# Kernel optimization log

Measured on AMD Instinct MI355X. Metric: run time of the kernel, lower is better.

The kernel has to match this reference:

```python
import jax, jax.numpy as jnp
import numpy as np

N_HEAD = 16
D_QK = 128
D_V = 128
D_MODEL = 2048
BATCH = 2
SEQ = 2048


def alibi_slopes(n_head):
    # standard ALiBi slopes: 2^(-8*i/n_head) for i = 1..n_head
    return jnp.asarray(2.0 ** (-8.0 * np.arange(1, n_head + 1) / n_head), dtype=jnp.float32)


def setup_inputs() -> dict:
    key = jax.random.key(0)
    k1, k2, k3, k4, k5 = jax.random.split(key, 5)
    x = jax.random.normal(k1, (BATCH, SEQ, D_MODEL), dtype=jnp.float32)
    # causal attention mask (1 = keep, 0 = masked), broadcast over heads
    causal = jnp.tril(jnp.ones((SEQ, SEQ), dtype=bool))
    attention_mask = jnp.broadcast_to(causal, (BATCH, 1, SEQ, SEQ))
    Wq = jax.random.normal(k2, (D_MODEL, N_HEAD * D_QK), dtype=jnp.float32) * (D_MODEL ** -0.5)
    Wk = jax.random.normal(k3, (D_MODEL, N_HEAD * D_QK), dtype=jnp.float32) * (D_MODEL ** -0.5)
    Wv = jax.random.normal(k4, (D_MODEL, N_HEAD * D_V), dtype=jnp.float32) * (D_MODEL ** -0.5)
    Wo = jax.random.normal(k5, (N_HEAD * D_V, D_MODEL), dtype=jnp.float32) * ((N_HEAD * D_V) ** -0.5)
    return {"x": x, "attention_mask": attention_mask, "Wq": Wq, "Wk": Wk, "Wv": Wv, "Wo": Wo}


def reference(x, attention_mask, Wq, Wk, Wv, Wo):
    B, S, _ = x.shape
    scale = D_QK ** -0.5
    q = (x @ Wq).reshape(B, S, N_HEAD, D_QK).transpose(0, 2, 1, 3)  # [B,H,S,dqk]
    k = (x @ Wk).reshape(B, S, N_HEAD, D_QK).transpose(0, 2, 1, 3)
    v = (x @ Wv).reshape(B, S, N_HEAD, D_V).transpose(0, 2, 1, 3)
    scores = jnp.einsum('bhid,bhjd->bhij', q, k) * scale  # [B,H,S,S]
    # ALiBi bias: slope_h * (j - i), negative penalty for distant past keys
    pos = jnp.arange(S, dtype=jnp.float32)
    rel = pos[None, :] - pos[:, None]  # [S,S]
    slopes = alibi_slopes(N_HEAD)
    scores = scores + slopes[None, :, None, None] * rel[None, None, :, :]
    scores = jnp.where(attention_mask, scores, jnp.float32(-jnp.inf))
    attn = jax.nn.softmax(scores, axis=-1)
    out = jnp.einsum('bhij,bhjd->bhid', attn, v)  # [B,H,S,dv]
    out = out.transpose(0, 2, 1, 3).reshape(B, S, N_HEAD * D_V)
    return out @ Wo
```

## Files before the change

kernel.cpp:

```cpp
#include <hip/hip_runtime.h>
#include <cstdint>

typedef unsigned short u16;
typedef __attribute__((ext_vector_type(4))) u16 u16x4;
typedef __attribute__((ext_vector_type(8))) u16 u16x8;
typedef __attribute__((ext_vector_type(8))) __bf16 bf16x8;
typedef __attribute__((ext_vector_type(4))) float f32x4;

#define LOG2E 1.44269504088896340736f

static __device__ __forceinline__ u16 f2bf(float f) {
  unsigned u = __builtin_bit_cast(unsigned, f);
  u += 0x7fffu + ((u >> 16) & 1u);
  return (u16)(u >> 16);
}
static __device__ __forceinline__ float bf2f(u16 v) {
  unsigned u = ((unsigned)v) << 16;
  return __builtin_bit_cast(float, u);
}


static __device__ __forceinline__ void gload16(const u16* g, u16* l) {
  __builtin_amdgcn_global_load_lds(
      (__attribute__((address_space(1))) void*)(uintptr_t)g,
      (__attribute__((address_space(3))) void*)(uintptr_t)l, 16, 0, 0);
}

static __device__ __forceinline__ bf16x8 lds_bf8(const void* p) {
  return __builtin_bit_cast(bf16x8, *(const u16x8*)p);
}

__global__ __launch_bounds__(256) void cast_x_kernel(const float* __restrict__ src,
                                                     u16* __restrict__ dst) {
  int i = (blockIdx.x * 256 + threadIdx.x) * 4;
  float4 v = *(const float4*)(src + i);
  u16x4 r = {f2bf(v.x), f2bf(v.y), f2bf(v.z), f2bf(v.w)};
  *(u16x4*)(dst + i) = r;
}

__global__ __launch_bounds__(256) void transpose_w4_kernel(const float* Wq, const float* Wk,
                                                           const float* Wv, const float* Wo,
                                                           u16* Wqt, u16* Wkt, u16* Wvt,
                                                           u16* Wot) {
  const float* src = blockIdx.z == 0 ? Wq : (blockIdx.z == 1 ? Wk : (blockIdx.z == 2 ? Wv : Wo));
  u16* dst = blockIdx.z == 0 ? Wqt : (blockIdx.z == 1 ? Wkt : (blockIdx.z == 2 ? Wvt : Wot));
  __shared__ float tile[32][33];
  const int n0 = blockIdx.x * 32, k0 = blockIdx.y * 32;
  const int tx = threadIdx.x & 31, ty = threadIdx.x >> 5;
#pragma unroll
  for (int r = 0; r < 4; ++r) {
    int row = r * 8 + ty;
    tile[row][tx] = src[(size_t)(k0 + row) * 2048 + n0 + tx];
  }
  __syncthreads();
#pragma unroll
  for (int r = 0; r < 4; ++r) {
    int row = r * 8 + ty;
    dst[(size_t)(n0 + row) * 2048 + k0 + tx] = f2bf(tile[tx][row]);
  }
}

#define GSTAGE(TILE, KH, BUF)                                                        \
  do {                                                                               \
    const int bk = (TILE) * 64 + (KH) * 32;                                          \
    u16* as_ = &lds[((BUF) * 2 + (KH)) * 8192];                                      \
    u16* bs_ = &lds[32768 + ((BUF) * 2 + (KH)) * BSLOT];                             \
    gload16(&A[(size_t)(m0 + sr) * 2048 + bk + scu], as_ + tid * 8);                 \
    gload16(&A[(size_t)(m0 + 128 + sr) * 2048 + bk + scu], as_ + 4096 + tid * 8);    \
    gload16(&Bt[(size_t)(n0 + sr) * 2048 + bk + scu], bs_ + tid * 8);                \
    if constexpr (BN == 256)                                                         \
      gload16(&Bt[(size_t)(n0 + 128 + sr) * 2048 + bk + scu], bs_ + 4096 + tid * 8); \
  } while (0)

#define GPH(BUF, KH, STAGE_STMT, VMLIT)                                              \
  do {                                                                               \
    const u16* as_ = &lds[((BUF) * 2 + (KH)) * 8192];                                \
    const u16* bs_ = &lds[32768 + ((BUF) * 2 + (KH)) * BSLOT];                       \
    bf16x8 af[8], bq[NF];                                                            \
    _Pragma("unroll") for (int mf = 0; mf < 8; ++mf) {                               \
      const int ar = wm * 128 + mf * 16 + l16;                                       \
      af[mf] = lds_bf8(&as_[(ar * 32 + lg * 8) ^ xsw]);                              \
    }                                                                                \
    _Pragma("unroll") for (int nf = 0; nf < NF; ++nf) {                              \
      const int br = wn * (BN / 4) + nf * 16 + l16;                                  \
      bq[nf] = lds_bf8(&bs_[(br * 32 + lg * 8) ^ xsw]);                              \
    }                                                                                \
    STAGE_STMT;                                                                      \
    asm volatile("s_barrier" ::: "memory");                                          \
    __builtin_amdgcn_s_setprio(1);                                                   \
    _Pragma("unroll") for (int mf = 0; mf < 8; ++mf)                                 \
        _Pragma("unroll") for (int nf = 0; nf < NF; ++nf) acc[mf][nf] =              \
            __builtin_amdgcn_mfma_f32_16x16x32_bf16(af[mf], bq[nf], acc[mf][nf], 0, 0, 0); \
    __builtin_amdgcn_s_setprio(0);                                                   \
    __builtin_amdgcn_sched_barrier(0);                                               \
    asm volatile("s_waitcnt vmcnt(" #VMLIT ")\n\ts_barrier" ::: "memory");           \
  } while (0)

template <int BN, int MODE>
__device__ __forceinline__ void gemm_dp(const u16* __restrict__ A, const u16* __restrict__ Bt,
                                        void* __restrict__ Cout, int m0, int n0) {
  constexpr int BSLOT = BN * 32;
  constexpr int NF = BN / 64;
  __shared__ u16 lds[32768 + 4 * BSLOT];
  const int tid = threadIdx.x, lane = tid & 63, w = tid >> 6;
  const int wm = w >> 2, wn = w & 3;
  const int l16 = lane & 15, lg = lane >> 4;
  const int sr = tid >> 2;
  const int scu = (((tid & 3) ^ ((tid >> 2) & 3))) * 8;
  const int xsw = (l16 & 3) * 8;

  f32x4 acc[8][NF];
#pragma unroll
  for (int i = 0; i < 8; ++i)
#pragma unroll
    for (int j = 0; j < NF; ++j) acc[i][j] = f32x4{0.f, 0.f, 0.f, 0.f};

  GSTAGE(0, 0, 0);
  GSTAGE(0, 1, 0);
  GSTAGE(1, 0, 1);
  if constexpr (BN == 256) {
    asm volatile("s_waitcnt vmcnt(8)\n\ts_barrier" ::: "memory");
    for (int m2 = 0; m2 < 30; m2 += 2) {
      GPH(0, 0, GSTAGE(m2 + 1, 1, 1), 8);
      GPH(0, 1, GSTAGE(m2 + 2, 0, 0), 8);
      GPH(1, 0, GSTAGE(m2 + 2, 1, 0), 8);
      GPH(1, 1, GSTAGE(m2 + 3, 0, 1), 8);
    }
    GPH(0, 0, GSTAGE(31, 1, 1), 8);
    GPH(0, 1, (void)0, 4);
    GPH(1, 0, (void)0, 0);
    GPH(1, 1, (void)0, 0);
  } else {
    asm volatile("s_waitcnt vmcnt(6)\n\ts_barrier" ::: "memory");
    for (int m2 = 0; m2 < 30; m2 += 2) {
      GPH(0, 0, GSTAGE(m2 + 1, 1, 1), 6);
      GPH(0, 1, GSTAGE(m2 + 2, 0, 0), 6);
      GPH(1, 0, GSTAGE(m2 + 2, 1, 0), 6);
      GPH(1, 1, GSTAGE(m2 + 3, 0, 1), 6);
    }
    GPH(0, 0, GSTAGE(31, 1, 1), 6);
    GPH(0, 1, (void)0, 3);
    GPH(1, 0, (void)0, 0);
    GPH(1, 1, (void)0, 0);
  }

  constexpr int WNS = BN / 4;
#pragma unroll
  for (int mf = 0; mf < 8; ++mf)
#pragma unroll
    for (int nf = 0; nf < NF; ++nf)
#pragma unroll
      for (int r = 0; r < 4; ++r) {
        const int row = m0 + wm * 128 + mf * 16 + lg * 4 + r;
        const int col = n0 + wn * WNS + nf * 16 + l16;
        const float v = acc[mf][nf][r];
        if constexpr (MODE == 0) {
          size_t off =
              (((size_t)(row >> 11) * 16 + (col >> 7)) * 2048 + (row & 2047)) * 128 + (col & 127);
          ((u16*)Cout)[off] = f2bf(v);
        } else if constexpr (MODE == 2) {
          size_t off =
              (((size_t)(col >> 11) * 16 + (row >> 7)) * 128 + (row & 127)) * 2048 + (col & 2047);
          ((u16*)Cout)[off] = f2bf(v);
        } else {
          ((float*)Cout)[(size_t)row * 2048 + col] = v;
        }
      }
}

__global__ __launch_bounds__(512, 2) void qkproj_kernel(const u16* xb, const u16* Wqt,
                                                        const u16* Wkt, u16* Qb, u16* Kb) {
  const int n0g = blockIdx.y * 256;
  const u16* Bt = (n0g < 2048) ? Wqt : Wkt;
  u16* dst = (n0g < 2048) ? Qb : Kb;
  gemm_dp<256, 0>(xb, Bt, dst, blockIdx.x * 256, n0g & 2047);
}

__global__ __launch_bounds__(512, 2) void vt_kernel(const u16* Wvt, const u16* xb, u16* Vb) {
  gemm_dp<128, 2>(Wvt, xb, Vb, blockIdx.x * 256, blockIdx.y * 128);
}

__global__ __launch_bounds__(512, 2) void out_kernel(const u16* OA, const u16* Wot, float* C) {
  gemm_dp<128, 1>(OA, Wot, C, blockIdx.x * 256, blockIdx.y * 128);
}

__global__ __launch_bounds__(256) void attn_kernel(const u16* __restrict__ Q,
                                                   const u16* __restrict__ Kg,
                                                   const u16* __restrict__ Vg,
                                                   u16* __restrict__ O,
                                                   u16* __restrict__ Opart,
                                                   float* __restrict__ Lp) {
  const int tid = threadIdx.x, lane = tid & 63, w = tid >> 6;
  const int l16 = lane & 15, lg = lane >> 4;

  const int u = blockIdx.x >> 5, bh = blockIdx.x & 31;
  int tile, st0, st1, slot = 0;
  bool multi = false;
  if (u == 0) { tile = 17; st0 = 0; st1 = 18; }
  else if (u == 1) { tile = 16; st0 = 0; st1 = 17; }
  else if (u < 30) {
    multi = true;
    const int c = u - 2, ti = c >> 1, ch = c & 1;
    tile = 31 - ti;
    const int s = tile + 1, half = (s + 1) >> 1;
    st0 = ch ? half : 0;
    st1 = ch ? s : half;
    slot = bh * 28 + c;
  } else { tile = 45 - u; st0 = 0; st1 = tile + 1; }

  const int q0 = tile * 64;
  const int h = bh & 15, b = bh >> 4;
  const float sl2 = exp2f(-0.5f * (float)(h + 1)) * LOG2E;
  const float sc2 = 0.08838834764831845f * LOG2E;

  __shared__ u16 Kl[64 * 128];
  __shared__ u16 Vl[128 * 64];
  __shared__ u16 Pl[64 * 64];

  const size_t qk_base = (size_t)bh * 2048 * 128;
  const size_t v_base = (size_t)bh * 128 * 2048;

  const u16* kgs = Kg + qk_base + (size_t)(tid >> 4) * 128 + (((tid & 15) ^ ((tid >> 4) & 7)) * 8);
  const u16* vgs = Vg + v_base + (size_t)(tid >> 3) * 2048 + (((tid & 7) ^ ((tid >> 3) & 7)) * 8);

#define STAGEKV(STX)                                                        \
  do {                                                                      \
    const int j0s = (STX)*64;                                               \
    _Pragma("unroll") for (int s = 0; s < 4; ++s) {                         \
      gload16(kgs + (size_t)(j0s + s * 16) * 128, Kl + s * 2048 + tid * 8); \
      gload16(vgs + (size_t)s * 32 * 2048 + j0s, Vl + s * 2048 + tid * 8);  \
    }                                                                       \
  } while (0)

  STAGEKV(st0);

  bf16x8 qf[4];
#pragma unroll
  for (int ks = 0; ks < 4; ++ks)
    qf[ks] = lds_bf8(&Q[qk_base + (size_t)(q0 + w * 16 + l16) * 128 + ks * 32 + lg * 8]);

  f32x4 oacc[8];
#pragma unroll
  for (int j = 0; j < 8; ++j) oacc[j] = f32x4{0.f, 0.f, 0.f, 0.f};
  float lsum0 = 0.f, lsum1 = 0.f;

  float ab4[4], rsl[4];
#pragma unroll
  for (int nf = 0; nf < 4; ++nf)
    ab4[nf] = (float)(st0 * 64 + nf * 16 - q0 - w * 16 - l16) * sl2;
#pragma unroll
  for (int r = 0; r < 4; ++r) rsl[r] = (float)(lg * 4 + r) * sl2;
  const float abinc = 64.0f * sl2;
  const int qrow = w * 16 + l16;
  const int dmaskb = lg * 4 - w * 16 - l16;

  __syncthreads();

#define ASTEP(MASKED)                                                                     \
  do {                                                                                    \
    f32x4 sacc[4];                                                                        \
    _Pragma("unroll") for (int j = 0; j < 4; ++j) sacc[j] = f32x4{0.f, 0.f, 0.f, 0.f};    \
    __builtin_amdgcn_s_setprio(1);                                                        \
    _Pragma("unroll") for (int ks = 0; ks < 4; ++ks) {                                    \
      bf16x8 kf[4];                                                                       \
      _Pragma("unroll") for (int nf = 0; nf < 4; ++nf) {                                  \
        int j = nf * 16 + l16;                                                            \
        kf[nf] = lds_bf8((char*)Kl + ((j * 256 + (ks * 32 + lg * 8) * 2) ^ ((j & 7) << 4))); \
      }                                                                                   \
      _Pragma("unroll") for (int nf = 0; nf < 4; ++nf) sacc[nf] =                         \
          __builtin_amdgcn_mfma_f32_16x16x32_bf16(kf[nf], qf[ks], sacc[nf], 0, 0, 0);     \
    }                                                                                     \
    __builtin_amdgcn_s_setprio(0);                                                        \
    _Pragma("unroll") for (int nf = 0; nf < 4; ++nf) {                                    \
      float pvv[4];                                                                       \
      _Pragma("unroll") for (int r = 0; r < 4; ++r) {                                     \
        float s2 = fmaf(sacc[nf][r], sc2, ab4[nf] + rsl[r]);                              \
        float pv = exp2f(s2);                                                             \
        if (MASKED) pv = (nf * 16 + r + dmaskb <= 0) ? pv : 0.f;                          \
        pvv[r] = pv;                                                                      \
      }                                                                                   \
      ab4[nf] += abinc;                                                                   \
      lsum0 += pvv[0] + pvv[1];                                                           \
      lsum1 += pvv[2] + pvv[3];                                                           \
      unsigned w0_, w1_;                                                                  \
      asm("v_cvt_pk_bf16_f32 %0, %1, %2" : "=v"(w0_) : "v"(pvv[0]), "v"(pvv[1]));         \
      asm("v_cvt_pk_bf16_f32 %0, %1, %2" : "=v"(w1_) : "v"(pvv[2]), "v"(pvv[3]));         \
      uint2 pw_{w0_, w1_};                                                                \
      *(uint2*)((char*)Pl + ((qrow * 128 + (nf * 16 + lg * 4) * 2) ^ ((qrow & 7) << 4))) = pw_; \
    }                                                                                     \
    __builtin_amdgcn_s_setprio(1);                                                        \
    _Pragma("unroll") for (int ks = 0; ks < 2; ++ks) {                                    \
      bf16x8 pf =                                                                         \
          lds_bf8((char*)Pl + ((qrow * 128 + (ks * 32 + lg * 8) * 2) ^ ((qrow & 7) << 4))); \
      _Pragma("unroll") for (int nf = 0; nf < 8; ++nf) {                                  \
        int d = nf * 16 + l16;                                                            \
        bf16x8 vf =                                                                       \
            lds_bf8((char*)Vl + ((d * 128 + (ks * 32 + lg * 8) * 2) ^ ((d & 7) << 4)));   \
        oacc[nf] = __builtin_amdgcn_mfma_f32_16x16x32_bf16(pf, vf, oacc[nf], 0, 0, 0);    \
      }                                                                                   \
    }                                                                                     \
    __builtin_amdgcn_s_setprio(0);                                                        \
    if (st + 1 < st1) {                                                                   \
      __syncthreads();                                                                    \
      STAGEKV(st + 1);                                                                    \
      __syncthreads();                                                                    \
    }                                                                                     \
  } while (0)

  int st = st0;
  const int bulk_end = min(st1, tile);
  for (; st < bulk_end; ++st) ASTEP(false);
  for (; st < st1; ++st) ASTEP(true);
#undef STAGEKV
#undef ASTEP

  float lr = lsum0 + lsum1;
  lr += __shfl_xor(lr, 16, 64);
  lr += __shfl_xor(lr, 32, 64);

  if (multi) {
    if (lg == 0) Lp[(size_t)slot * 64 + qrow] = lr;
#pragma unroll
    for (int r = 0; r < 4; ++r) {
      const int row = w * 16 + lg * 4 + r;
#pragma unroll
      for (int nf = 0; nf < 8; ++nf)
        Opart[((size_t)slot * 64 + row) * 128 + nf * 16 + l16] = f2bf(oacc[nf][r]);
    }
  } else {
#pragma unroll
    for (int r = 0; r < 4; ++r) {
      const float inv = 1.0f / __shfl(lr, lg * 4 + r, 64);
      const int srow = q0 + w * 16 + lg * 4 + r;
#pragma unroll
      for (int nf = 0; nf < 8; ++nf)
        O[((size_t)b * 2048 + srow) * 2048 + h * 128 + nf * 16 + l16] = f2bf(oacc[nf][r] * inv);
    }
  }
}

__global__ __launch_bounds__(256) void combine_kernel(const u16* __restrict__ Opart,
                                                      const float* __restrict__ Lp,
                                                      u16* __restrict__ O) {
  const int bx = blockIdx.x;
  const int bh = bx / 14, ti = bx % 14;
  const int tile = 31 - ti;
  const int slot0 = bh * 28 + ti * 2, slot1 = slot0 + 1;
  const int b = bh >> 4, h = bh & 15;
  const int q0 = tile * 64;
  const int tid = threadIdx.x;
  const int colg = (tid & 15) * 8, rowb = tid >> 4;
#pragma unroll
  for (int rr = 0; rr < 4; ++rr) {
    const int row = rowb + rr * 16;
    const float l0 = Lp[(size_t)slot0 * 64 + row];
    const float l1 = Lp[(size_t)slot1 * 64 + row];
    const float inv = 1.0f / (l0 + l1);
    u16x8 p0 = *(const u16x8*)&Opart[((size_t)slot0 * 64 + row) * 128 + colg];
    u16x8 p1 = *(const u16x8*)&Opart[((size_t)slot1 * 64 + row) * 128 + colg];
    u16x8 o;
#pragma unroll
    for (int e = 0; e < 8; ++e) o[e] = f2bf((bf2f(p0[e]) + bf2f(p1[e])) * inv);
    *(u16x8*)&O[((size_t)b * 2048 + q0 + row) * 2048 + h * 128 + colg] = o;
  }
}

extern "C" void kernel_launch(void* const* d_in, const int* in_sizes, int n_in, void* d_out,
                              int out_size, void* d_ws, size_t ws_size, hipStream_t stream) {
  const float* x = (const float*)d_in[0];
  const float* Wq = (const float*)d_in[2];
  const float* Wk = (const float*)d_in[3];
  const float* Wv = (const float*)d_in[4];
  const float* Wo = (const float*)d_in[5];
  char* ws = (char*)d_ws;

  const size_t MB = 1048576;
  u16* xb = (u16*)(ws);
  u16* Qb = (u16*)(ws + 16 * MB);
  u16* Kb = (u16*)(ws + 32 * MB);
  u16* Vb = (u16*)(ws + 48 * MB);
  u16* Wqt = (u16*)(ws + 64 * MB);
  u16* Wkt = (u16*)(ws + 72 * MB);
  u16* Wvt = (u16*)(ws + 80 * MB);
  u16* Wot = (u16*)(ws + 88 * MB);
  u16* OA = xb;
  u16* Opart = (u16*)(ws + 72 * MB);
  float* Lpf = (float*)(ws + 72 * MB + 896ull * 64 * 128 * 2);

  cast_x_kernel<<<8192, 256, 0, stream>>>(x, xb);
  transpose_w4_kernel<<<dim3(64, 64, 4), 256, 0, stream>>>(Wq, Wk, Wv, Wo, Wqt, Wkt, Wvt, Wot);
  qkproj_kernel<<<dim3(16, 16), 512, 0, stream>>>(xb, Wqt, Wkt, Qb, Kb);
  vt_kernel<<<dim3(8, 32), 512, 0, stream>>>(Wvt, xb, Vb);
  attn_kernel<<<dim3(1472), 256, 0, stream>>>(Qb, Kb, Vb, OA, Opart, Lpf);
  combine_kernel<<<dim3(448), 256, 0, stream>>>(Opart, Lpf, OA);
  out_kernel<<<dim3(16, 16), 512, 0, stream>>>(OA, Wot, (float*)d_out);
}
```

Before: 251.9 us.

## Give BN=128 GEMMs a three-stage 64-wide K pipeline with 8-way swizzle

The QK projection kernel is specialised inline for BN=256. The V-transpose and output-projection GEMMs move to a new gemm_dp2 path. That path stages full 64-wide K tiles into a three-buffer ring (144KB LDS) with an 8-column XOR swizzle, and each wave issues 32 MFMAs per phase instead of 16. The goal is fewer barriers per K step and deeper prefetch to hide global latency. The cost is occupancy: launch bounds drop to one block per CU because of the larger LDS footprint.

```diff
diff --git a/kernel.cpp b/kernel.cpp
--- a/kernel.cpp
+++ b/kernel.cpp
@@ -64,44 +64,48 @@
   do {                                                                               \
     const int bk = (TILE) * 64 + (KH) * 32;                                          \
     u16* as_ = &lds[((BUF) * 2 + (KH)) * 8192];                                      \
-    u16* bs_ = &lds[32768 + ((BUF) * 2 + (KH)) * BSLOT];                             \
+    u16* bs_ = &lds[32768 + ((BUF) * 2 + (KH)) * 8192];                              \
     gload16(&A[(size_t)(m0 + sr) * 2048 + bk + scu], as_ + tid * 8);                 \
     gload16(&A[(size_t)(m0 + 128 + sr) * 2048 + bk + scu], as_ + 4096 + tid * 8);    \
     gload16(&Bt[(size_t)(n0 + sr) * 2048 + bk + scu], bs_ + tid * 8);                \
-    if constexpr (BN == 256)                                                         \
-      gload16(&Bt[(size_t)(n0 + 128 + sr) * 2048 + bk + scu], bs_ + 4096 + tid * 8); \
+    gload16(&Bt[(size_t)(n0 + 128 + sr) * 2048 + bk + scu], bs_ + 4096 + tid * 8);   \
   } while (0)
 
 #define GPH(BUF, KH, STAGE_STMT, VMLIT)                                              \
   do {                                                                               \
     const u16* as_ = &lds[((BUF) * 2 + (KH)) * 8192];                                \
-    const u16* bs_ = &lds[32768 + ((BUF) * 2 + (KH)) * BSLOT];                       \
-    bf16x8 af[8], bq[NF];                                                            \
+    const u16* bs_ = &lds[32768 + ((BUF) * 2 + (KH)) * 8192];                        \
+    bf16x8 af[8], bq[4];                                                             \
     _Pragma("unroll") for (int mf = 0; mf < 8; ++mf) {                               \
       const int ar = wm * 128 + mf * 16 + l16;                                       \
       af[mf] = lds_bf8(&as_[(ar * 32 + lg * 8) ^ xsw]);                              \
     }                                                                                \
-    _Pragma("unroll") for (int nf = 0; nf < NF; ++nf) {                              \
-      const int br = wn * (BN / 4) + nf * 16 + l16;                                  \
+    _Pragma("unroll") for (int nf = 0; nf < 4; ++nf) {                               \
+      const int br = wn * 64 + nf * 16 + l16;                                        \
       bq[nf] = lds_bf8(&bs_[(br * 32 + lg * 8) ^ xsw]);                              \
     }                                                                                \
     STAGE_STMT;                                                                      \
     asm volatile("s_barrier" ::: "memory");                                          \
     __builtin_amdgcn_s_setprio(1);                                                   \
     _Pragma("unroll") for (int mf = 0; mf < 8; ++mf)                                 \
-        _Pragma("unroll") for (int nf = 0; nf < NF; ++nf) acc[mf][nf] =              \
+        _Pragma("unroll") for (int nf = 0; nf < 4; ++nf) acc[mf][nf] =               \
             __builtin_amdgcn_mfma_f32_16x16x32_bf16(af[mf], bq[nf], acc[mf][nf], 0, 0, 0); \
     __builtin_amdgcn_s_setprio(0);                                                   \
     __builtin_amdgcn_sched_barrier(0);                                               \
     asm volatile("s_waitcnt vmcnt(" #VMLIT ")\n\ts_barrier" ::: "memory");           \
   } while (0)
 
-template <int BN, int MODE>
-__device__ __forceinline__ void gemm_dp(const u16* __restrict__ A, const u16* __restrict__ Bt,
-                                        void* __restrict__ Cout, int m0, int n0) {
-  constexpr int BSLOT = BN * 32;
-  constexpr int NF = BN / 64;
-  __shared__ u16 lds[32768 + 4 * BSLOT];
+__global__ __launch_bounds__(512, 2) void qkproj_kernel(const u16* __restrict__ xb,
+                                                        const u16* __restrict__ Wqt,
+                                                        const u16* __restrict__ Wkt,
+                                                        u16* __restrict__ Qb,
+                                                        u16* __restrict__ Kb) {
+  const int n0g = blockIdx.y * 256;
+  const u16* Bt = (n0g < 2048) ? Wqt : Wkt;
+  u16* Cout = (n0g < 2048) ? Qb : Kb;
+  const u16* A = xb;
+  const int m0 = blockIdx.x * 256, n0 = n0g & 2047;
+  __shared__ u16 lds[65536];
   const int tid = threadIdx.x, lane = tid & 63, w = tid >> 6;
   const int wm = w >> 2, wn = w & 3;
   const int l16 = lane & 15, lg = lane >> 4;
@@ -109,56 +113,120 @@
   const int scu = (((tid & 3) ^ ((tid >> 2) & 3))) * 8;
   const int xsw = (l16 & 3) * 8;
 
-  f32x4 acc[8][NF];
+  f32x4 acc[8][4];
 #pragma unroll
   for (int i = 0; i < 8; ++i)
 #pragma unroll
-    for (int j = 0; j < NF; ++j) acc[i][j] = f32x4{0.f, 0.f, 0.f, 0.f};
+    for (int j = 0; j < 4; ++j) acc[i][j] = f32x4{0.f, 0.f, 0.f, 0.f};
 
   GSTAGE(0, 0, 0);
   GSTAGE(0, 1, 0);
   GSTAGE(1, 0, 1);
-  if constexpr (BN == 256) {
-    asm volatile("s_waitcnt vmcnt(8)\n\ts_barrier" ::: "memory");
-    for (int m2 = 0; m2 < 30; m2 += 2) {
-      GPH(0, 0, GSTAGE(m2 + 1, 1, 1), 8);
-      GPH(0, 1, GSTAGE(m2 + 2, 0, 0), 8);
-      GPH(1, 0, GSTAGE(m2 + 2, 1, 0), 8);
-      GPH(1, 1, GSTAGE(m2 + 3, 0, 1), 8);
-    }
-    GPH(0, 0, GSTAGE(31, 1, 1), 8);
-    GPH(0, 1, (void)0, 4);
-    GPH(1, 0, (void)0, 0);
-    GPH(1, 1, (void)0, 0);
-  } else {
-    asm volatile("s_waitcnt vmcnt(6)\n\ts_barrier" ::: "memory");
-    for (int m2 = 0; m2 < 30; m2 += 2) {
-      GPH(0, 0, GSTAGE(m2 + 1, 1, 1), 6);
-      GPH(0, 1, GSTAGE(m2 + 2, 0, 0), 6);
-      GPH(1, 0, GSTAGE(m2 + 2, 1, 0), 6);
-      GPH(1, 1, GSTAGE(m2 + 3, 0, 1), 6);
-    }
-    GPH(0, 0, GSTAGE(31, 1, 1), 6);
-    GPH(0, 1, (void)0, 3);
-    GPH(1, 0, (void)0, 0);
-    GPH(1, 1, (void)0, 0);
-  }
-
-  constexpr int WNS = BN / 4;
+  asm volatile("s_waitcnt vmcnt(8)\n\ts_barrier" ::: "memory");
+  for (int m2 = 0; m2 < 30; m2 += 2) {
+    GPH(0, 0, GSTAGE(m2 + 1, 1, 1), 8);
+    GPH(0, 1, GSTAGE(m2 + 2, 0, 0), 8);
+    GPH(1, 0, GSTAGE(m2 + 2, 1, 0), 8);
+    GPH(1, 1, GSTAGE(m2 + 3, 0, 1), 8);
+  }
+  GPH(0, 0, GSTAGE(31, 1, 1), 8);
+  GPH(0, 1, (void)0, 4);
+  GPH(1, 0, (void)0, 0);
+  GPH(1, 1, (void)0, 0);
+
 #pragma unroll
   for (int mf = 0; mf < 8; ++mf)
 #pragma unroll
-    for (int nf = 0; nf < NF; ++nf)
+    for (int nf = 0; nf < 4; ++nf)
 #pragma unroll
       for (int r = 0; r < 4; ++r) {
         const int row = m0 + wm * 128 + mf * 16 + lg * 4 + r;
-        const int col = n0 + wn * WNS + nf * 16 + l16;
+        const int col = n0 + wn * 64 + nf * 16 + l16;
+        size_t off =
+            (((size_t)(row >> 11) * 16 + (col >> 7)) * 2048 + (row & 2047)) * 128 + (col & 127);
+        Cout[off] = f2bf(acc[mf][nf][r]);
+      }
+}
+
+#define GSTAGE2(TILE, S)                                                             \
+  do {                                                                               \
+    const int bk2 = (TILE) * 64;                                                     \
+    u16* as_ = &lds[(S) * 16384];                                                    \
+    u16* bs_ = &lds[49152 + (S) * 8192];                                             \
+    gload16(pA2 + bk2, as_ + tid * 8);                                               \
+    gload16(pA2 + bk2 + (size_t)64 * 2048, as_ + 4096 + tid * 8);                    \
+    gload16(pA2 + bk2 + (size_t)128 * 2048, as_ + 8192 + tid * 8);                   \
+    gload16(pA2 + bk2 + (size_t)192 * 2048, as_ + 12288 + tid * 8);                  \
+    gload16(pB2 + bk2, bs_ + tid * 8);                                               \
+    gload16(pB2 + bk2 + (size_t)64 * 2048, bs_ + 4096 + tid * 8);                    \
+  } while (0)
+
+#define GPH2(S, STAGE_STMT, VMLIT)                                                   \
+  do {                                                                               \
+    const char* as_ = (const char*)&lds[(S) * 16384];                                \
+    const char* bs_ = (const char*)&lds[49152 + (S) * 8192];                         \
+    bf16x8 af[2][8], bq[2][2];                                                       \
+    _Pragma("unroll") for (int kh = 0; kh < 2; ++kh)                                 \
+        _Pragma("unroll") for (int mf = 0; mf < 8; ++mf) {                           \
+      const int ar = wm * 128 + mf * 16 + l16;                                       \
+      af[kh][mf] = lds_bf8(as_ + ((ar * 128 + (kh * 4 + lg) * 16) ^ ((l16 & 7) << 4))); \
+    }                                                                                \
+    _Pragma("unroll") for (int kh = 0; kh < 2; ++kh)                                 \
+        _Pragma("unroll") for (int nf = 0; nf < 2; ++nf) {                           \
+      const int br = wn * 32 + nf * 16 + l16;                                        \
+      bq[kh][nf] = lds_bf8(bs_ + ((br * 128 + (kh * 4 + lg) * 16) ^ ((l16 & 7) << 4))); \
+    }                                                                                \
+    STAGE_STMT;                                                                      \
+    asm volatile("s_barrier" ::: "memory");                                          \
+    __builtin_amdgcn_s_setprio(1);                                                   \
+    _Pragma("unroll") for (int kh = 0; kh < 2; ++kh)                                 \
+        _Pragma("unroll") for (int mf = 0; mf < 8; ++mf)                             \
+            _Pragma("unroll") for (int nf = 0; nf < 2; ++nf) acc[mf][nf] =           \
+                __builtin_amdgcn_mfma_f32_16x16x32_bf16(af[kh][mf], bq[kh][nf],      \
+                                                        acc[mf][nf], 0, 0, 0);      \
+    __builtin_amdgcn_s_setprio(0);                                                   \
+    __builtin_amdgcn_sched_barrier(0);                                               \
+    asm volatile("s_waitcnt vmcnt(" #VMLIT ")\n\ts_barrier" ::: "memory");           \
+  } while (0)
+
+template <int MODE>
+__device__ __forceinline__ void gemm_dp2(const u16* __restrict__ A, const u16* __restrict__ Bt,
+                                         void* __restrict__ Cout, int m0, int n0) {
+  __shared__ u16 lds[73728];
+  const int tid = threadIdx.x, lane = tid & 63, w = tid >> 6;
+  const int wm = w >> 2, wn = w & 3;
+  const int l16 = lane & 15, lg = lane >> 4;
+  const int scol2 = ((tid & 7) ^ ((tid >> 3) & 7)) * 8;
+  const u16* pA2 = A + (size_t)(m0 + (tid >> 3)) * 2048 + scol2;
+  const u16* pB2 = Bt + (size_t)(n0 + (tid >> 3)) * 2048 + scol2;
+
+  f32x4 acc[8][2];
+#pragma unroll
+  for (int i = 0; i < 8; ++i)
+#pragma unroll
+    for (int j = 0; j < 2; ++j) acc[i][j] = f32x4{0.f, 0.f, 0.f, 0.f};
+
+  GSTAGE2(0, 0);
+  GSTAGE2(1, 1);
+  asm volatile("s_waitcnt vmcnt(6)\n\ts_barrier" ::: "memory");
+  for (int t = 0; t < 30; t += 3) {
+    GPH2(0, GSTAGE2(t + 2, 2), 6);
+    GPH2(1, GSTAGE2(t + 3, 0), 6);
+    GPH2(2, GSTAGE2(t + 4, 1), 6);
+  }
+  GPH2(0, (void)0, 0);
+  GPH2(1, (void)0, 0);
+
+#pragma unroll
+  for (int mf = 0; mf < 8; ++mf)
+#pragma unroll
+    for (int nf = 0; nf < 2; ++nf)
+#pragma unroll
+      for (int r = 0; r < 4; ++r) {
+        const int row = m0 + wm * 128 + mf * 16 + lg * 4 + r;
+        const int col = n0 + wn * 32 + nf * 16 + l16;
         const float v = acc[mf][nf][r];
-        if constexpr (MODE == 0) {
-          size_t off =
-              (((size_t)(row >> 11) * 16 + (col >> 7)) * 2048 + (row & 2047)) * 128 + (col & 127);
-          ((u16*)Cout)[off] = f2bf(v);
-        } else if constexpr (MODE == 2) {
+        if constexpr (MODE == 2) {
           size_t off =
               (((size_t)(col >> 11) * 16 + (row >> 7)) * 128 + (row & 127)) * 2048 + (col & 2047);
           ((u16*)Cout)[off] = f2bf(v);
@@ -168,20 +236,12 @@
       }
 }
 
-__global__ __launch_bounds__(512, 2) void qkproj_kernel(const u16* xb, const u16* Wqt,
-                                                        const u16* Wkt, u16* Qb, u16* Kb) {
-  const int n0g = blockIdx.y * 256;
-  const u16* Bt = (n0g < 2048) ? Wqt : Wkt;
-  u16* dst = (n0g < 2048) ? Qb : Kb;
-  gemm_dp<256, 0>(xb, Bt, dst, blockIdx.x * 256, n0g & 2047);
-}
-
-__global__ __launch_bounds__(512, 2) void vt_kernel(const u16* Wvt, const u16* xb, u16* Vb) {
-  gemm_dp<128, 2>(Wvt, xb, Vb, blockIdx.x * 256, blockIdx.y * 128);
-}
-
-__global__ __launch_bounds__(512, 2) void out_kernel(const u16* OA, const u16* Wot, float* C) {
-  gemm_dp<128, 1>(OA, Wot, C, blockIdx.x * 256, blockIdx.y * 128);
+__global__ __launch_bounds__(512, 1) void vt_kernel(const u16* Wvt, const u16* xb, u16* Vb) {
+  gemm_dp2<2>(Wvt, xb, Vb, blockIdx.x * 256, blockIdx.y * 128);
+}
+
+__global__ __launch_bounds__(512, 1) void out_kernel(const u16* OA, const u16* Wot, float* C) {
+  gemm_dp2<1>(OA, Wot, C, blockIdx.x * 256, blockIdx.y * 128);
 }
 
 __global__ __launch_bounds__(256) void attn_kernel(const u16* __restrict__ Q,
```

New measurement: 241.3 us. 1.04x faster.
